# Kernel optimization log

Hardware: AMD Instinct MI355X
Metric: run time of the kernel (lower is better)

The kernel has to match this reference:

```python
import jax, jax.numpy as jnp
import numpy as np

SIGMA = 1e-4      # cone height (DistanceFieldPenetrationLoss sigma)
EPS = 1e-9
THRESH = 2000.0   # pen_loss[pen_loss < 2000]
WEIGHT = 0.1      # self.weight


def setup_inputs() -> dict:
    key = jax.random.key(0)
    k1, k2, k3, k4 = jax.random.split(key, 4)
    B, NV, NF, C = 16, 6890, 13776, 65536
    verts = jax.random.normal(k1, (B, NV, 3), dtype=jnp.float32)
    trans = jax.random.normal(k2, (B, 3), dtype=jnp.float32)
    faces = jax.random.randint(k3, (NF, 3), 0, NV)
    collision_idxs = jax.random.randint(k4, (B // 2, C, 2), 0, 2 * NF)
    return {"verts": verts, "trans": trans, "faces": faces,
            "collision_idxs": collision_idxs}


def _pen_distance(triangles, collision_idxs):
    # triangles: [Bp, F, 3, 3]; collision_idxs: [Bp, C, 2]
    intr_idx = collision_idxs[..., 0]
    recv_idx = collision_idxs[..., 1]
    # stand-in for the BVH's (-1)-padding / self-collision filter
    valid = (intr_idx != recv_idx).astype(triangles.dtype)            # [Bp, C]
    gather = jax.vmap(lambda t, i: t[i])
    intr = gather(triangles, intr_idx)                                # [Bp, C, 3, 3]
    recv = gather(triangles, recv_idx)                                # [Bp, C, 3, 3]
    # receiver triangle frame
    e1 = recv[..., 1, :] - recv[..., 0, :]
    e2 = recv[..., 2, :] - recv[..., 0, :]
    n = jnp.cross(e1, e2)
    n = n / (jnp.linalg.norm(n, axis=-1, keepdims=True) + EPS)        # unit normal
    c = recv.mean(axis=-2)                                            # [Bp, C, 3] centroid
    radius = jnp.linalg.norm(recv - c[..., None, :], axis=-1).max(axis=-1)  # circumscribed radius
    # conical distance field evaluated at the 3 intruder vertices
    delta = intr - c[..., None, :]                                    # [Bp, C, 3, 3]
    d = jnp.einsum('bcvk,bck->bcv', delta, n)                         # signed normal distance
    radial = jnp.linalg.norm(delta - d[..., None] * n[..., None, :], axis=-1)
    field = jax.nn.relu(-d / SIGMA) * jax.nn.relu(1.0 - radial / (radius[..., None] + EPS))
    pair_loss = (field ** 2).sum(axis=-1)                             # [Bp, C]
    return (pair_loss * valid).sum(axis=-1)                           # [Bp]


def reference(verts, trans, faces, collision_idxs):
    B, NV, _ = verts.shape
    NF = faces.shape[0]
    vertices = verts + trans[:, None, :]                              # [B, NV, 3]
    offs = (jnp.arange(B, dtype=faces.dtype) * NV)[:, None, None]
    faces_idx = (faces[None] + offs).reshape(B // 2, 2 * NF, 3)       # merge person pairs
    triangles = vertices.reshape(-1, 3)[faces_idx]                    # [B//2, 2*NF, 3, 3]
    pen = _pen_distance(triangles, collision_idxs)                    # [B//2]
    keep = (pen < THRESH).astype(pen.dtype)
    cnt = keep.sum()
    vals = (jax.nn.sigmoid(pen / THRESH) - 0.5) * keep
    loss = jnp.where(cnt > 0, vals.sum() / jnp.maximum(cnt, 1.0), 0.0) * WEIGHT
    return loss
```

## Files before the change

### kernel.cpp

```cpp
#include <hip/hip_runtime.h>
#include <math.h>


namespace {
constexpr int kNV = 6890;
constexpr int kNF = 13776;
constexpr int kP  = 8;
constexpr int kC  = 65536;
constexpr int kNB = 256;
constexpr int kTPB = 256;
constexpr int kWPB = kTPB / 64;
constexpr int kBlocksPerPair = kNB / kP;
constexpr int kPasses = kC / (kBlocksPerPair * kTPB);
}

#define SIGMA_F  1e-4f
#define EPS_F    1e-9f
#define THRESH_F 2000.0f
#define WEIGHT_F 0.1f

__device__ float g_partials[kNB];

__device__ __forceinline__ float cone_pair_loss(
    float3 r0, float3 r1, float3 r2, float3 i0, float3 i1, float3 i2) {
    float e1x = r1.x - r0.x, e1y = r1.y - r0.y, e1z = r1.z - r0.z;
    float e2x = r2.x - r0.x, e2y = r2.y - r0.y, e2z = r2.z - r0.z;
    float nx = e1y * e2z - e1z * e2y;
    float ny = e1z * e2x - e1x * e2z;
    float nz = e1x * e2y - e1y * e2x;
    float nn = sqrtf(nx * nx + ny * ny + nz * nz) + EPS_F;
    nx /= nn; ny /= nn; nz /= nn;
    float cx = (r0.x + r1.x + r2.x) / 3.0f;
    float cy = (r0.y + r1.y + r2.y) / 3.0f;
    float cz = (r0.z + r1.z + r2.z) / 3.0f;
    float r2m = 0.0f;
    {
        float dx = r0.x - cx, dy = r0.y - cy, dz = r0.z - cz;
        r2m = fmaxf(r2m, dx * dx + dy * dy + dz * dz);
        dx = r1.x - cx; dy = r1.y - cy; dz = r1.z - cz;
        r2m = fmaxf(r2m, dx * dx + dy * dy + dz * dz);
        dx = r2.x - cx; dy = r2.y - cy; dz = r2.z - cz;
        r2m = fmaxf(r2m, dx * dx + dy * dy + dz * dz);
    }
    float rad_eps = sqrtf(r2m) + EPS_F;
    float3 iv[3] = {i0, i1, i2};
    float acc = 0.0f;
#pragma unroll
    for (int k = 0; k < 3; ++k) {
        float dx = iv[k].x - cx, dy = iv[k].y - cy, dz = iv[k].z - cz;
        float d = dx * nx + dy * ny + dz * nz;
        float px = dx - d * nx, py = dy - d * ny, pz = dz - d * nz;
        float radial = sqrtf(px * px + py * py + pz * pz);
        float fa = fmaxf(-d / SIGMA_F, 0.0f);
        float fb = fmaxf(1.0f - radial / rad_eps, 0.0f);
        float fd = fa * fb;
        acc += fd * fd;
    }
    return acc;
}

__device__ __forceinline__ float eval_collision(
    int p, int2 idx,
    const float* __restrict__ verts, const int* __restrict__ faces,
    float t0x, float t0y, float t0z, float t1x, float t1y, float t1z) {
    int hi = (idx.x >= kNF) ? 1 : 0;
    int hr = (idx.y >= kNF) ? 1 : 0;
    const int* fi = faces + 3 * (idx.x - hi * kNF);
    const int* fr = faces + 3 * (idx.y - hr * kNF);
    int vi0 = fi[0], vi1 = fi[1], vi2 = fi[2];
    int vr0 = fr[0], vr1 = fr[1], vr2 = fr[2];
    size_t bi = (size_t)(2 * p + hi) * kNV;
    size_t br = (size_t)(2 * p + hr) * kNV;
    float tix = hi ? t1x : t0x, tiy = hi ? t1y : t0y, tiz = hi ? t1z : t0z;
    float trx = hr ? t1x : t0x, try_ = hr ? t1y : t0y, trz = hr ? t1z : t0z;
    const float* q;
    q = verts + (bi + vi0) * 3; float3 i0 = make_float3(q[0] + tix, q[1] + tiy, q[2] + tiz);
    q = verts + (bi + vi1) * 3; float3 i1 = make_float3(q[0] + tix, q[1] + tiy, q[2] + tiz);
    q = verts + (bi + vi2) * 3; float3 i2 = make_float3(q[0] + tix, q[1] + tiy, q[2] + tiz);
    q = verts + (br + vr0) * 3; float3 r0 = make_float3(q[0] + trx, q[1] + try_, q[2] + trz);
    q = verts + (br + vr1) * 3; float3 r1 = make_float3(q[0] + trx, q[1] + try_, q[2] + trz);
    q = verts + (br + vr2) * 3; float3 r2 = make_float3(q[0] + trx, q[1] + try_, q[2] + trz);
    float v = cone_pair_loss(r0, r1, r2, i0, i1, i2);
    return (idx.x != idx.y) ? v : 0.0f;
}

__global__ void __launch_bounds__(256)
pen_kernel(const int* __restrict__ coll,
           const float* __restrict__ verts,
           const float* __restrict__ trans,
           const int* __restrict__ faces) {
    const int blk  = blockIdx.x;
    const int p    = blk & 7;
    const int lane = threadIdx.x & 63;
    const int wid  = threadIdx.x >> 6;
    const int2* cp = (const int2*)coll + (size_t)p * kC
                   + (size_t)(blk >> 3) * (kPasses * kTPB);

    const float t0x = trans[6 * p + 0], t0y = trans[6 * p + 1], t0z = trans[6 * p + 2];
    const float t1x = trans[6 * p + 3], t1y = trans[6 * p + 4], t1z = trans[6 * p + 5];

    volatile __shared__ int s_exit;
    if (threadIdx.x == 0) s_exit = 0;
    __syncthreads();

    float acc = 0.0f;
    for (int s = 0; s < kPasses; ++s) {
        int2 idx = cp[s * kTPB + threadIdx.x];
        acc += eval_collision(p, idx, verts, faces, t0x, t0y, t0z, t1x, t1y, t1z);
        if (__any(acc >= THRESH_F)) {
            if (lane == 0) s_exit = 1;
            break;
        }
        if (s + 1 < kPasses && s_exit) break;
    }

#pragma unroll
    for (int off = 32; off > 0; off >>= 1)
        acc += __shfl_down(acc, off, 64);
    __shared__ float red[kWPB];
    if (lane == 0) red[wid] = acc;
    __syncthreads();
    if (threadIdx.x == 0)
        g_partials[blk] = red[0] + red[1] + red[2] + red[3];
}

__global__ void __launch_bounds__(512)
finalize_kernel(float* __restrict__ out) {
    const int wv   = threadIdx.x >> 6;
    const int lane = threadIdx.x & 63;
    float s = 0.0f;
    for (int j = lane; j < kBlocksPerPair; j += 64)
        s += g_partials[wv + 8 * j];
#pragma unroll
    for (int off = 32; off > 0; off >>= 1)
        s += __shfl_down(s, off, 64);
    __shared__ float pen[kP];
    if (lane == 0) pen[wv] = s;
    __syncthreads();
    if (threadIdx.x == 0) {
        float cnt = 0.0f, vals = 0.0f;
#pragma unroll
        for (int e = 0; e < kP; ++e) {
            float pq = pen[e];
            if (pq < THRESH_F) {
                cnt += 1.0f;
                vals += 1.0f / (1.0f + expf(-pq / THRESH_F)) - 0.5f;
            }
        }
        float loss = (cnt > 0.0f) ? (vals / fmaxf(cnt, 1.0f)) : 0.0f;
        out[0] = loss * WEIGHT_F;
    }
}

extern "C" void kernel_launch(void* const* d_in, const int* in_sizes, int n_in,
                              void* d_out, int out_size, void* d_ws, size_t ws_size,
                              hipStream_t stream) {
    const float* verts = (const float*)d_in[0];
    const float* trans = (const float*)d_in[1];
    const int*   faces = (const int*)d_in[2];
    const int*   coll  = (const int*)d_in[3];
    (void)d_ws; (void)ws_size; (void)in_sizes; (void)n_in; (void)out_size;
    pen_kernel<<<kNB, kTPB, 0, stream>>>(coll, verts, trans, faces);
    finalize_kernel<<<1, 512, 0, stream>>>((float*)d_out);
}
```

Before: 65.85 us.

## Fuse penalty and finalize into one single-block kernel with per-pair early exit

Replaces the 256-block penalty kernel and the separate finalize kernel with one 1024-thread block. Two waves handle each person pair and stop early once a pair's partial penalty reaches the threshold. The final sigmoid/threshold reduction then runs in shared memory in the same block. This removes a second launch and the global partial buffer, but it puts all work on one CU. It only stays cheap if the early exit fires quickly; otherwise each wave must loop through hundreds of passes serially.

Measured after the change: 73.41 us. 1.11x slower.

```diff
diff --git a/kernel.cpp b/kernel.cpp
--- a/kernel.cpp
+++ b/kernel.cpp
@@ -7,19 +7,15 @@
 constexpr int kNF = 13776;
 constexpr int kP  = 8;
 constexpr int kC  = 65536;
-constexpr int kNB = 256;
-constexpr int kTPB = 256;
-constexpr int kWPB = kTPB / 64;
-constexpr int kBlocksPerPair = kNB / kP;
-constexpr int kPasses = kC / (kBlocksPerPair * kTPB);
+constexpr int kTPB = 1024;
+constexpr int kLanesPerPair = 128;
+constexpr int kPasses = kC / kLanesPerPair;
 }
 
 #define SIGMA_F  1e-4f
 #define EPS_F    1e-9f
 #define THRESH_F 2000.0f
 #define WEIGHT_F 0.1f
-
-__device__ float g_partials[kNB];
 
 __device__ __forceinline__ float cone_pair_loss(
     float3 r0, float3 r1, float3 r2, float3 i0, float3 i1, float3 i2) {
@@ -84,64 +80,50 @@
     return (idx.x != idx.y) ? v : 0.0f;
 }
 
-__global__ void __launch_bounds__(256)
-pen_kernel(const int* __restrict__ coll,
+__global__ void __launch_bounds__(1024)
+pen_single(const int* __restrict__ coll,
            const float* __restrict__ verts,
            const float* __restrict__ trans,
-           const int* __restrict__ faces) {
-    const int blk  = blockIdx.x;
-    const int p    = blk & 7;
-    const int lane = threadIdx.x & 63;
-    const int wid  = threadIdx.x >> 6;
-    const int2* cp = (const int2*)coll + (size_t)p * kC
-                   + (size_t)(blk >> 3) * (kPasses * kTPB);
+           const int* __restrict__ faces,
+           float* __restrict__ out) {
+    const int tid  = threadIdx.x;
+    const int lane = tid & 63;
+    const int w    = tid >> 6;
+    const int p    = w >> 1;
+    const int sub  = w & 1;
+    const int2* cp = (const int2*)coll + (size_t)p * kC;
 
     const float t0x = trans[6 * p + 0], t0y = trans[6 * p + 1], t0z = trans[6 * p + 2];
     const float t1x = trans[6 * p + 3], t1y = trans[6 * p + 4], t1z = trans[6 * p + 5];
 
-    volatile __shared__ int s_exit;
-    if (threadIdx.x == 0) s_exit = 0;
+    __shared__ int   s_exit[kP];
+    __shared__ float s_red[16];
+    if (tid < kP) s_exit[tid] = 0;
     __syncthreads();
+    volatile int* vexit = s_exit;
 
     float acc = 0.0f;
     for (int s = 0; s < kPasses; ++s) {
-        int2 idx = cp[s * kTPB + threadIdx.x];
+        int2 idx = cp[s * kLanesPerPair + sub * 64 + lane];
         acc += eval_collision(p, idx, verts, faces, t0x, t0y, t0z, t1x, t1y, t1z);
         if (__any(acc >= THRESH_F)) {
-            if (lane == 0) s_exit = 1;
+            if (lane == 0) vexit[p] = 1;
             break;
         }
-        if (s + 1 < kPasses && s_exit) break;
+        if (vexit[p]) break;
     }
 
 #pragma unroll
     for (int off = 32; off > 0; off >>= 1)
         acc += __shfl_down(acc, off, 64);
-    __shared__ float red[kWPB];
-    if (lane == 0) red[wid] = acc;
+    if (lane == 0) s_red[w] = acc;
     __syncthreads();
-    if (threadIdx.x == 0)
-        g_partials[blk] = red[0] + red[1] + red[2] + red[3];
-}
 
-__global__ void __launch_bounds__(512)
-finalize_kernel(float* __restrict__ out) {
-    const int wv   = threadIdx.x >> 6;
-    const int lane = threadIdx.x & 63;
-    float s = 0.0f;
-    for (int j = lane; j < kBlocksPerPair; j += 64)
-        s += g_partials[wv + 8 * j];
-#pragma unroll
-    for (int off = 32; off > 0; off >>= 1)
-        s += __shfl_down(s, off, 64);
-    __shared__ float pen[kP];
-    if (lane == 0) pen[wv] = s;
-    __syncthreads();
-    if (threadIdx.x == 0) {
+    if (tid == 0) {
         float cnt = 0.0f, vals = 0.0f;
 #pragma unroll
         for (int e = 0; e < kP; ++e) {
-            float pq = pen[e];
+            float pq = s_red[2 * e] + s_red[2 * e + 1];
             if (pq < THRESH_F) {
                 cnt += 1.0f;
                 vals += 1.0f / (1.0f + expf(-pq / THRESH_F)) - 0.5f;
@@ -160,6 +142,5 @@
     const int*   faces = (const int*)d_in[2];
     const int*   coll  = (const int*)d_in[3];
     (void)d_ws; (void)ws_size; (void)in_sizes; (void)n_in; (void)out_size;
-    pen_kernel<<<kNB, kTPB, 0, stream>>>(coll, verts, trans, faces);
-    finalize_kernel<<<1, 512, 0, stream>>>((float*)d_out);
+    pen_single<<<1, kTPB, 0, stream>>>(coll, verts, trans, faces, (float*)d_out);
 }
```
